# Performance work log

Measured on AMD Instinct MI355X. Metric: run time of the kernel, lower is better.

The kernel has to match this reference:

```python
import jax, jax.numpy as jnp
import numpy as np

POOL_D, POOL_H, POOL_W = 4, 7, 7
SPATIAL_SCALE = 0.25
SAMPLING_RATIO = 2


def setup_inputs() -> dict:
    key = jax.random.key(0)
    k1, k2, k3, k4 = jax.random.split(key, 4)
    N, C, D, H, W = 2, 128, 32, 64, 64
    features = jax.random.normal(k1, (N, C, D, H, W), dtype=jnp.float32)
    R = 256
    inv = 1.0 / SPATIAL_SCALE  # rois live in image coords; features at stride 4
    batch = jax.random.randint(k2, (R,), 0, N).astype(jnp.float32)
    dims = jnp.array([D, H, W], dtype=jnp.float32)
    starts = jax.random.uniform(k3, (R, 3)) * dims * inv * 0.6
    sizes = (0.1 + 0.3 * jax.random.uniform(k4, (R, 3))) * dims * inv
    z1, y1, x1 = starts[:, 0], starts[:, 1], starts[:, 2]
    z2, y2, x2 = z1 + sizes[:, 0], y1 + sizes[:, 1], x1 + sizes[:, 2]
    # roi layout: (batch_idx, x1, y1, z1, x2, y2, z2)
    rois = jnp.stack([batch, x1, y1, z1, x2, y2, z2], axis=1).astype(jnp.float32)
    return {"features": features, "rois": rois}


def _axis(coords, size):
    # classic RoIAlign border handling: outside [-1, size] -> 0 contribution
    valid = (coords >= -1.0) & (coords <= float(size))
    c = jnp.clip(coords, 0.0, float(size) - 1.0)
    lo = jnp.floor(c)
    hi = jnp.minimum(lo + 1.0, float(size) - 1.0)
    w = c - lo  # weight of the hi corner
    return lo.astype(jnp.int32), hi.astype(jnp.int32), w, valid


def roi_align_3d(features, rois):
    N, C, D, H, W = features.shape
    R = rois.shape[0]
    sr = SAMPLING_RATIO
    b = rois[:, 0].astype(jnp.int32)
    x1 = rois[:, 1] * SPATIAL_SCALE
    y1 = rois[:, 2] * SPATIAL_SCALE
    z1 = rois[:, 3] * SPATIAL_SCALE
    x2 = rois[:, 4] * SPATIAL_SCALE
    y2 = rois[:, 5] * SPATIAL_SCALE
    z2 = rois[:, 6] * SPATIAL_SCALE
    rd = jnp.maximum(z2 - z1, 1.0)
    rh = jnp.maximum(y2 - y1, 1.0)
    rw = jnp.maximum(x2 - x1, 1.0)

    def sample_coords(start, extent, P):
        # sampling_ratio sample centers per output bin -> [R, P*sr]
        t = (jnp.arange(P * sr, dtype=jnp.float32) + 0.5) / sr
        return start[:, None] + t[None, :] * (extent / P)[:, None]

    zs = sample_coords(z1, rd, POOL_D)  # [R, SD]
    ys = sample_coords(y1, rh, POOL_H)  # [R, SH]
    xs = sample_coords(x1, rw, POOL_W)  # [R, SW]
    zlo, zhi, wz, vz = _axis(zs, D)
    ylo, yhi, wy, vy = _axis(ys, H)
    xlo, xhi, wx, vx = _axis(xs, W)

    B = b[:, None, None, None]
    Z = lambda a: a[:, :, None, None]
    Y = lambda a: a[:, None, :, None]
    X = lambda a: a[:, None, None, :]

    def g(zi, yi, xi):
        # gather -> [R, SD, SH, SW, C]
        return features[B, :, Z(zi), Y(yi), X(xi)]

    wz1, wy1, wx1 = Z(wz)[..., None], Y(wy)[..., None], X(wx)[..., None]
    wz0, wy0, wx0 = 1.0 - wz1, 1.0 - wy1, 1.0 - wx1
    val = (g(zlo, ylo, xlo) * (wz0 * wy0 * wx0)
           + g(zlo, ylo, xhi) * (wz0 * wy0 * wx1)
           + g(zlo, yhi, xlo) * (wz0 * wy1 * wx0)
           + g(zlo, yhi, xhi) * (wz0 * wy1 * wx1)
           + g(zhi, ylo, xlo) * (wz1 * wy0 * wx0)
           + g(zhi, ylo, xhi) * (wz1 * wy0 * wx1)
           + g(zhi, yhi, xlo) * (wz1 * wy1 * wx0)
           + g(zhi, yhi, xhi) * (wz1 * wy1 * wx1))
    valid = (Z(vz) & Y(vy) & X(vx))[..., None]
    val = jnp.where(valid, val, 0.0)
    # average the sr^3 samples per bin
    val = val.reshape(R, POOL_D, sr, POOL_H, sr, POOL_W, sr, C)
    out = val.mean(axis=(2, 4, 6))  # [R, PD, PH, PW, C]
    return jnp.transpose(out, (0, 4, 1, 2, 3))  # [R, C, PD, PH, PW]


def reference(features, rois):
    return roi_align_3d(features, rois)
```

## Files before the change

### kernel.cpp

```cpp
#include <hip/hip_runtime.h>

constexpr int C_  = 128;
constexpr int D_  = 32;
constexpr int H_  = 64;
constexpr int W_  = 64;
constexpr int PD = 4;
constexpr int PH = 7;
constexpr int PW = 7;
constexpr int SR = 2;
constexpr float SCALE = 0.25f;
constexpr int S_ = D_ * H_ * W_;
constexpr int BINS_PER_ROI = PD * PH * PW;
constexpr int SLAB = PH * PW;

typedef float vf4 __attribute__((ext_vector_type(4)));
typedef float f32x2 __attribute__((ext_vector_type(2)));

__device__ __forceinline__ void axis2(float start, float extent, int P, int p,
                                      int size, int lo[2], int hi[2],
                                      float w[2], bool v[2]) {
    float bin = extent / (float)P;
#pragma unroll
    for (int u = 0; u < 2; ++u) {
        float t = ((float)(p * SR + u) + 0.5f) / (float)SR;
        float coord = start + t * bin;
        v[u] = (coord >= -1.0f) && (coord <= (float)size);
        float cc = fminf(fmaxf(coord, 0.0f), (float)size - 1.0f);
        float fl = floorf(cc);
        lo[u] = (int)fl;
        hi[u] = min(lo[u] + 1, size - 1);
        w[u] = cc - fl;
    }
}

struct AxisW {
    int base;
    float w[4];
};

__device__ __forceinline__ AxisW axis_merge(float start, float extent, int P,
                                            int p, int size) {
    const float bin = extent / (float)P;
    const float t0 = ((float)(p * SR) + 0.5f) / (float)SR;
    const float c0 = start + t0 * bin;
    const float va = (c0 >= -1.0f && c0 <= (float)size) ? 1.0f : 0.0f;
    const float cc0 = fminf(fmaxf(c0, 0.0f), (float)size - 1.0f);
    const float fl0 = floorf(cc0);
    const int lo0 = (int)fl0;
    const int hi0 = min(lo0 + 1, size - 1);
    const float f0 = cc0 - fl0;
    const float a0 = (1.0f - f0) * va;
    const float a1 = f0 * va;
    const float t1 = ((float)(p * SR + 1) + 0.5f) / (float)SR;
    const float c1 = start + t1 * bin;
    const float vb = (c1 >= -1.0f && c1 <= (float)size) ? 1.0f : 0.0f;
    const float cc1 = fminf(fmaxf(c1, 0.0f), (float)size - 1.0f);
    const float fl1 = floorf(cc1);
    const int lo1 = (int)fl1;
    const int hi1 = min(lo1 + 1, size - 1);
    const float f1 = cc1 - fl1;
    const float b0 = (1.0f - f1) * vb;
    const float b1 = f1 * vb;

    const int dh0 = hi0 - lo0;
    const int dl1 = lo1 - lo0;
    const int dh1 = hi1 - lo0;

    float w0 = a0, w1 = 0.f, w2 = 0.f, w3 = 0.f;
    if (dh0 == 0) w0 += a1; else w1 += a1;
    w0 += (dl1 == 0) ? b0 : 0.f;
    w1 += (dl1 == 1) ? b0 : 0.f;
    w2 += (dl1 == 2) ? b0 : 0.f;
    w0 += (dh1 == 0) ? b1 : 0.f;
    w1 += (dh1 == 1) ? b1 : 0.f;
    w2 += (dh1 == 2) ? b1 : 0.f;
    w3 += (dh1 == 3) ? b1 : 0.f;

    AxisW r;
    r.base = lo0;
    r.w[0] = w0; r.w[1] = w1; r.w[2] = w2; r.w[3] = w3;
    return r;
}

__device__ __forceinline__ unsigned int f2bf(float f) {
    unsigned int u = __float_as_uint(f);
    u += 0x7fffu + ((u >> 16) & 1u);
    return u >> 16;
}

__global__ __launch_bounds__(512) void transpose_bf16(
    const float* __restrict__ in, unsigned int* __restrict__ outp) {
    __shared__ unsigned int tileu[256][64];
    const int n  = blockIdx.y;
    const int s0 = blockIdx.x * 256;
    const int t  = threadIdx.x;

    const float* src = in + (size_t)n * C_ * S_;
    unsigned int* dst = outp + (size_t)n * (C_ / 2) * S_;

    if (n == 0 && blockIdx.x == 0 && t < 256) {
        outp[(size_t)gridDim.y * (C_ / 2) * S_ + t] = 0u;
    }

    {
        const int sl  = t & 63;
        const int cp0 = t >> 6;
#pragma unroll
        for (int p = 0; p < 8; ++p) {
            const int cp = cp0 + 8 * p;
            const int c = cp * 2;
            const vf4 a = __builtin_nontemporal_load(
                (const vf4*)&src[(size_t)c * S_ + (s0 + 4 * sl)]);
            const vf4 b = __builtin_nontemporal_load(
                (const vf4*)&src[(size_t)(c + 1) * S_ + (s0 + 4 * sl)]);
            const int col = cp ^ (sl & 31);
            tileu[4 * sl + 0][col] = f2bf(a.x) | (f2bf(b.x) << 16);
            tileu[4 * sl + 1][col] = f2bf(a.y) | (f2bf(b.y) << 16);
            tileu[4 * sl + 2][col] = f2bf(a.z) | (f2bf(b.z) << 16);
            tileu[4 * sl + 3][col] = f2bf(a.w) | (f2bf(b.w) << 16);
        }
    }
    __syncthreads();
    {
        const int cp2   = (t & 31) * 2;
        const int rbase = t >> 5;
#pragma unroll
        for (int it = 0; it < 16; ++it) {
            const int s = rbase + 16 * it;
            const int w = (s >> 2) & 31;
            uint2 v;
            v.x = tileu[s][cp2 ^ w];
            v.y = tileu[s][(cp2 + 1) ^ w];
            *(uint2*)&dst[(size_t)(s0 + s) * (C_ / 2) + cp2] = v;
        }
    }
}

__global__ __launch_bounds__(448, 7) void roi_align_slot(
    const unsigned short* __restrict__ ft,
    const float* __restrict__ rois,
    float* __restrict__ out,
    int R) {
    __shared__ float tile[7][128];

    int roi, pd, part;
    {
        const int B = blockIdx.x;
        if ((R & 7) == 0) {
            const int xcd = B & 7;
            const int j = B >> 3;
            roi = xcd + 8 * (j / 28);
            const int sub = j % 28;
            pd = sub / 7;
            part = sub - pd * 7;
        } else {
            roi = B / 28;
            const int sub = B - roi * 28;
            pd = sub / 7;
            part = sub - pd * 7;
        }
    }

    const int t = threadIdx.x;
    const int w = t >> 6;
    const int lane = t & 63;
    const int slot = part * 7 + w;

    const float* roip = rois + (size_t)roi * 7;
    const int b = (int)roip[0];
    const float x1 = roip[1] * SCALE, y1 = roip[2] * SCALE, z1 = roip[3] * SCALE;
    const float x2 = roip[4] * SCALE, y2 = roip[5] * SCALE, z2 = roip[6] * SCALE;
    const float rd = fmaxf(z2 - z1, 1.0f);
    const float rh = fmaxf(y2 - y1, 1.0f);
    const float rw = fmaxf(x2 - x1, 1.0f);

    AxisW az = axis_merge(z1, rd, PD, pd, D_);
    {
        const float s = 1.0f / (SR * SR * SR);
        az.w[0] *= s; az.w[1] *= s; az.w[2] *= s; az.w[3] *= s;
    }

    const int ph = slot / PW;
    const int pw = slot - ph * PW;
    const AxisW ay = axis_merge(y1, rh, PH, ph, H_);
    const AxisW ax = axis_merge(x1, rw, PW, pw, W_);

    int zw[4], yw[4];
#pragma unroll
    for (int i = 0; i < 4; ++i) {
        zw[i] = __builtin_amdgcn_readfirstlane((int)__float_as_uint(az.w[i]));
        yw[i] = __builtin_amdgcn_readfirstlane((int)__float_as_uint(ay.w[i]));
    }

    const int v = lane >> 4;
    float wxl = ax.w[0];
    wxl = (v == 1) ? ax.w[1] : wxl;
    wxl = (v == 2) ? ax.w[2] : wxl;
    wxl = (v == 3) ? ax.w[3] : wxl;

    unsigned yoff[4];
#pragma unroll
    for (int iy = 0; iy < 4; ++iy) {
        const int yy = min(ay.base + iy, H_ - 1);
        yoff[iy] = ((unsigned)yy * W_ + (unsigned)ax.base) * C_;
    }
    unsigned zrow[4];
#pragma unroll
    for (int iz = 0; iz < 4; ++iz) {
        const int zz = min(az.base + iz, D_ - 1);
        zrow[iz] = (((unsigned)b * D_ + (unsigned)zz) * H_) *
                   (unsigned)(W_ * C_);
    }

    const unsigned short* lanep = ft + (unsigned)lane * 8;

    f32x2 acc2[4];
#pragma unroll
    for (int j = 0; j < 4; ++j) { acc2[j].x = 0.f; acc2[j].y = 0.f; }

    uint4 q[8];
#pragma unroll
    for (int zb = 0; zb < 2; ++zb) {
        if (zb == 1) {
            __builtin_amdgcn_sched_barrier(0);
        }
#pragma unroll
        for (int dz = 0; dz < 2; ++dz) {
            const int iz = 2 * zb + dz;
            if (zw[iz] == 0) continue;
#pragma unroll
            for (int iy = 0; iy < 4; ++iy) {
                if (yw[iy] == 0) continue;
                q[dz * 4 + iy] = *(const uint4*)(lanep + zrow[iz] + yoff[iy]);
            }
        }
#pragma unroll
        for (int dz = 0; dz < 2; ++dz) {
            const int iz = 2 * zb + dz;
            if (zw[iz] == 0) continue;
#pragma unroll
            for (int iy = 0; iy < 4; ++iy) {
                if (yw[iy] == 0) continue;
                const float wf = (az.w[iz] * ay.w[iy]) * wxl;
                f32x2 wf2; wf2.x = wf; wf2.y = wf;
                const uint4 qq = q[dz * 4 + iy];
                f32x2 p;
                p.x = __uint_as_float(qq.x << 16);
                p.y = __uint_as_float(qq.x & 0xffff0000u);
                acc2[0] = __builtin_elementwise_fma(p, wf2, acc2[0]);
                p.x = __uint_as_float(qq.y << 16);
                p.y = __uint_as_float(qq.y & 0xffff0000u);
                acc2[1] = __builtin_elementwise_fma(p, wf2, acc2[1]);
                p.x = __uint_as_float(qq.z << 16);
                p.y = __uint_as_float(qq.z & 0xffff0000u);
                acc2[2] = __builtin_elementwise_fma(p, wf2, acc2[2]);
                p.x = __uint_as_float(qq.w << 16);
                p.y = __uint_as_float(qq.w & 0xffff0000u);
                acc2[3] = __builtin_elementwise_fma(p, wf2, acc2[3]);
            }
        }
    }

#pragma unroll
    for (int j = 0; j < 4; ++j) {
        float sx = acc2[j].x;
        sx += __shfl_xor(sx, 16);
        sx += __shfl_xor(sx, 32);
        float sy = acc2[j].y;
        sy += __shfl_xor(sy, 16);
        sy += __shfl_xor(sy, 32);
        if (lane < 16) {
            tile[w][lane * 8 + 2 * j]     = sx;
            tile[w][lane * 8 + 2 * j + 1] = sy;
        }
    }

    __syncthreads();

    const size_t obase =
        (size_t)roi * C_ * BINS_PER_ROI + (size_t)pd * SLAB + (size_t)part * 7;
#pragma unroll
    for (int it = 0; it < 2; ++it) {
        const int idx = t + it * 448;
        const int c = idx / 7;
        const int o = idx - c * 7;
        __builtin_nontemporal_store(tile[o][c],
                                    &out[obase + (size_t)c * BINS_PER_ROI + o]);
    }
}

__global__ void roi_align_direct(const float* __restrict__ feat,
                                 const float* __restrict__ rois,
                                 float* __restrict__ out, int total) {
    const int tid = blockIdx.x * blockDim.x + threadIdx.x;
    if (tid >= total) return;
    int t = tid;
    const int pw = t % PW; t /= PW;
    const int ph = t % PH; t /= PH;
    const int pd = t % PD; t /= PD;
    const int c = t % C_;  t /= C_;
    const int r = t;

    const float* roi = rois + (size_t)r * 7;
    const int b = (int)roi[0];
    const float x1 = roi[1] * SCALE, y1 = roi[2] * SCALE, z1 = roi[3] * SCALE;
    const float x2 = roi[4] * SCALE, y2 = roi[5] * SCALE, z2 = roi[6] * SCALE;
    const float rd = fmaxf(z2 - z1, 1.0f);
    const float rh = fmaxf(y2 - y1, 1.0f);
    const float rw = fmaxf(x2 - x1, 1.0f);

    int zlo[2], zhi[2], ylo[2], yhi[2], xlo[2], xhi[2];
    float wz[2], wy[2], wx[2];
    bool vz[2], vy[2], vx[2];
    axis2(z1, rd, PD, pd, D_, zlo, zhi, wz, vz);
    axis2(y1, rh, PH, ph, H_, ylo, yhi, wy, vy);
    axis2(x1, rw, PW, pw, W_, xlo, xhi, wx, vx);

    const float* fc = feat + ((size_t)b * C_ + c) * S_;
    float acc = 0.0f;
#pragma unroll
    for (int i = 0; i < 2; ++i) {
        if (!vz[i]) continue;
#pragma unroll
        for (int j = 0; j < 2; ++j) {
            if (!vy[j]) continue;
            const size_t r00 = ((size_t)zlo[i] * H_ + ylo[j]) * W_;
            const size_t r10 = ((size_t)zhi[i] * H_ + ylo[j]) * W_;
            const size_t r01 = ((size_t)zlo[i] * H_ + yhi[j]) * W_;
            const size_t r11 = ((size_t)zhi[i] * H_ + yhi[j]) * W_;
            const float wz1 = wz[i], wz0 = 1.0f - wz1;
            const float wy1 = wy[j], wy0 = 1.0f - wy1;
#pragma unroll
            for (int k = 0; k < 2; ++k) {
                if (!vx[k]) continue;
                const float wx1 = wx[k], wx0 = 1.0f - wx1;
                acc += wz0 * (wy0 * (wx0 * fc[r00 + xlo[k]] + wx1 * fc[r00 + xhi[k]]) +
                              wy1 * (wx0 * fc[r01 + xlo[k]] + wx1 * fc[r01 + xhi[k]])) +
                       wz1 * (wy0 * (wx0 * fc[r10 + xlo[k]] + wx1 * fc[r10 + xhi[k]]) +
                              wy1 * (wx0 * fc[r11 + xlo[k]] + wx1 * fc[r11 + xhi[k]]));
            }
        }
    }
    out[tid] = acc * (1.0f / (SR * SR * SR));
}

extern "C" void kernel_launch(void* const* d_in, const int* in_sizes, int n_in,
                              void* d_out, int out_size, void* d_ws,
                              size_t ws_size, hipStream_t stream) {
    const float* features = (const float*)d_in[0];
    const float* rois = (const float*)d_in[1];
    float* out = (float*)d_out;

    const int R = in_sizes[1] / 7;
    const int N = in_sizes[0] / (C_ * S_);
    const size_t need = (size_t)in_sizes[0] * sizeof(unsigned short) + 1024;

    if (ws_size >= need) {
        unsigned short* ft = (unsigned short*)d_ws;

        dim3 tg(S_ / 256, N);
        transpose_bf16<<<tg, 512, 0, stream>>>(features, (unsigned int*)ft);

        roi_align_slot<<<R * PD * 7, 448, 0, stream>>>(ft, rois, out, R);
    } else {
        const int total = R * C_ * BINS_PER_ROI;
        roi_align_direct<<<(total + 255) / 256, 256, 0, stream>>>(
            features, rois, out, total);
    }
}
```

Measured before the change: 251.1 us.

## Process a full PH×PW slab per block, looping over ph inside each wave

Each block now handles a whole (roi, pd) slab of 49 bins, and each wave loops over all 7 ph rows for a fixed pw column, instead of one block per 7 bins. The grid shrinks by a factor of seven, the per-block roi and z-axis setup is shared across more work, and output stores become contiguous 49-float runs per channel. The cost is fewer blocks (1024) with more serial work per wave and a larger shared tile, which may reduce latency hiding for the gather loads. The transpose kernel is unchanged and still runs every call.

Measured after the change: 284.0 us. +13.1%, slower.

```diff
diff --git a/kernel.cpp b/kernel.cpp
--- a/kernel.cpp
+++ b/kernel.cpp
@@ -38,9 +38,8 @@
     float w[4];
 };
 
-__device__ __forceinline__ AxisW axis_merge(float start, float extent, int P,
-                                            int p, int size) {
-    const float bin = extent / (float)P;
+__device__ __forceinline__ AxisW axis_merge_bin(float start, float bin, int p,
+                                                int size) {
     const float t0 = ((float)(p * SR) + 0.5f) / (float)SR;
     const float c0 = start + t0 * bin;
     const float va = (c0 >= -1.0f && c0 <= (float)size) ? 1.0f : 0.0f;
@@ -82,6 +81,11 @@
     return r;
 }
 
+__device__ __forceinline__ AxisW axis_merge(float start, float extent, int P,
+                                            int p, int size) {
+    return axis_merge_bin(start, extent / (float)P, p, size);
+}
+
 __device__ __forceinline__ unsigned int f2bf(float f) {
     unsigned int u = __float_as_uint(f);
     u += 0x7fffu + ((u >> 16) & 1u);
@@ -136,35 +140,30 @@
     }
 }
 
-__global__ __launch_bounds__(448, 7) void roi_align_slot(
+__global__ __launch_bounds__(448, 7) void roi_align_slab7(
     const unsigned short* __restrict__ ft,
     const float* __restrict__ rois,
     float* __restrict__ out,
     int R) {
-    __shared__ float tile[7][128];
-
-    int roi, pd, part;
+    __shared__ float tile[SLAB][132];
+
+    int roi, pd;
     {
         const int B = blockIdx.x;
         if ((R & 7) == 0) {
             const int xcd = B & 7;
             const int j = B >> 3;
-            roi = xcd + 8 * (j / 28);
-            const int sub = j % 28;
-            pd = sub / 7;
-            part = sub - pd * 7;
+            roi = xcd + 8 * (j >> 2);
+            pd = j & 3;
         } else {
-            roi = B / 28;
-            const int sub = B - roi * 28;
-            pd = sub / 7;
-            part = sub - pd * 7;
+            roi = B >> 2;
+            pd = B & 3;
         }
     }
 
     const int t = threadIdx.x;
     const int w = t >> 6;
     const int lane = t & 63;
-    const int slot = part * 7 + w;
 
     const float* roip = rois + (size_t)roi * 7;
     const int b = (int)roip[0];
@@ -179,18 +178,13 @@
         const float s = 1.0f / (SR * SR * SR);
         az.w[0] *= s; az.w[1] *= s; az.w[2] *= s; az.w[3] *= s;
     }
-
-    const int ph = slot / PW;
-    const int pw = slot - ph * PW;
-    const AxisW ay = axis_merge(y1, rh, PH, ph, H_);
-    const AxisW ax = axis_merge(x1, rw, PW, pw, W_);
-
-    int zw[4], yw[4];
-#pragma unroll
-    for (int i = 0; i < 4; ++i) {
+    const AxisW ax = axis_merge(x1, rw, PW, w, W_);
+    const float biny = rh / (float)PH;
+
+    int zw[4];
+#pragma unroll
+    for (int i = 0; i < 4; ++i)
         zw[i] = __builtin_amdgcn_readfirstlane((int)__float_as_uint(az.w[i]));
-        yw[i] = __builtin_amdgcn_readfirstlane((int)__float_as_uint(ay.w[i]));
-    }
 
     const int v = lane >> 4;
     float wxl = ax.w[0];
@@ -198,12 +192,6 @@
     wxl = (v == 2) ? ax.w[2] : wxl;
     wxl = (v == 3) ? ax.w[3] : wxl;
 
-    unsigned yoff[4];
-#pragma unroll
-    for (int iy = 0; iy < 4; ++iy) {
-        const int yy = min(ay.base + iy, H_ - 1);
-        yoff[iy] = ((unsigned)yy * W_ + (unsigned)ax.base) * C_;
-    }
     unsigned zrow[4];
 #pragma unroll
     for (int iz = 0; iz < 4; ++iz) {
@@ -214,76 +202,91 @@
 
     const unsigned short* lanep = ft + (unsigned)lane * 8;
 
-    f32x2 acc2[4];
-#pragma unroll
-    for (int j = 0; j < 4; ++j) { acc2[j].x = 0.f; acc2[j].y = 0.f; }
-
-    uint4 q[8];
-#pragma unroll
-    for (int zb = 0; zb < 2; ++zb) {
-        if (zb == 1) {
-            __builtin_amdgcn_sched_barrier(0);
-        }
-#pragma unroll
-        for (int dz = 0; dz < 2; ++dz) {
-            const int iz = 2 * zb + dz;
-            if (zw[iz] == 0) continue;
-#pragma unroll
-            for (int iy = 0; iy < 4; ++iy) {
-                if (yw[iy] == 0) continue;
-                q[dz * 4 + iy] = *(const uint4*)(lanep + zrow[iz] + yoff[iy]);
+#pragma unroll
+    for (int ph = 0; ph < PH; ++ph) {
+        const AxisW ay = axis_merge_bin(y1, biny, ph, H_);
+        int yw[4];
+#pragma unroll
+        for (int i = 0; i < 4; ++i)
+            yw[i] = __builtin_amdgcn_readfirstlane(
+                (int)__float_as_uint(ay.w[i]));
+        unsigned yoff[4];
+#pragma unroll
+        for (int iy = 0; iy < 4; ++iy) {
+            const int yy = min(ay.base + iy, H_ - 1);
+            yoff[iy] = ((unsigned)yy * W_ + (unsigned)ax.base) * C_;
+        }
+
+        f32x2 acc2[4];
+#pragma unroll
+        for (int j = 0; j < 4; ++j) { acc2[j].x = 0.f; acc2[j].y = 0.f; }
+
+        uint4 q[8];
+#pragma unroll
+        for (int zb = 0; zb < 2; ++zb) {
+            if (zb == 1) __builtin_amdgcn_sched_barrier(0);
+#pragma unroll
+            for (int dz = 0; dz < 2; ++dz) {
+                const int iz = 2 * zb + dz;
+                if (zw[iz] == 0) continue;
+#pragma unroll
+                for (int iy = 0; iy < 4; ++iy) {
+                    if (yw[iy] == 0) continue;
+                    q[dz * 4 + iy] =
+                        *(const uint4*)(lanep + zrow[iz] + yoff[iy]);
+                }
             }
-        }
-#pragma unroll
-        for (int dz = 0; dz < 2; ++dz) {
-            const int iz = 2 * zb + dz;
-            if (zw[iz] == 0) continue;
-#pragma unroll
-            for (int iy = 0; iy < 4; ++iy) {
-                if (yw[iy] == 0) continue;
-                const float wf = (az.w[iz] * ay.w[iy]) * wxl;
-                f32x2 wf2; wf2.x = wf; wf2.y = wf;
-                const uint4 qq = q[dz * 4 + iy];
-                f32x2 p;
-                p.x = __uint_as_float(qq.x << 16);
-                p.y = __uint_as_float(qq.x & 0xffff0000u);
-                acc2[0] = __builtin_elementwise_fma(p, wf2, acc2[0]);
-                p.x = __uint_as_float(qq.y << 16);
-                p.y = __uint_as_float(qq.y & 0xffff0000u);
-                acc2[1] = __builtin_elementwise_fma(p, wf2, acc2[1]);
-                p.x = __uint_as_float(qq.z << 16);
-                p.y = __uint_as_float(qq.z & 0xffff0000u);
-                acc2[2] = __builtin_elementwise_fma(p, wf2, acc2[2]);
-                p.x = __uint_as_float(qq.w << 16);
-                p.y = __uint_as_float(qq.w & 0xffff0000u);
-                acc2[3] = __builtin_elementwise_fma(p, wf2, acc2[3]);
+#pragma unroll
+            for (int dz = 0; dz < 2; ++dz) {
+                const int iz = 2 * zb + dz;
+                if (zw[iz] == 0) continue;
+#pragma unroll
+                for (int iy = 0; iy < 4; ++iy) {
+                    if (yw[iy] == 0) continue;
+                    const float wf = (az.w[iz] * ay.w[iy]) * wxl;
+                    f32x2 wf2; wf2.x = wf; wf2.y = wf;
+                    const uint4 qq = q[dz * 4 + iy];
+                    f32x2 p;
+                    p.x = __uint_as_float(qq.x << 16);
+                    p.y = __uint_as_float(qq.x & 0xffff0000u);
+                    acc2[0] = __builtin_elementwise_fma(p, wf2, acc2[0]);
+                    p.x = __uint_as_float(qq.y << 16);
+                    p.y = __uint_as_float(qq.y & 0xffff0000u);
+                    acc2[1] = __builtin_elementwise_fma(p, wf2, acc2[1]);
+                    p.x = __uint_as_float(qq.z << 16);
+                    p.y = __uint_as_float(qq.z & 0xffff0000u);
+                    acc2[2] = __builtin_elementwise_fma(p, wf2, acc2[2]);
+                    p.x = __uint_as_float(qq.w << 16);
+                    p.y = __uint_as_float(qq.w & 0xffff0000u);
+                    acc2[3] = __builtin_elementwise_fma(p, wf2, acc2[3]);
+                }
             }
         }
-    }
-
-#pragma unroll
-    for (int j = 0; j < 4; ++j) {
-        float sx = acc2[j].x;
-        sx += __shfl_xor(sx, 16);
-        sx += __shfl_xor(sx, 32);
-        float sy = acc2[j].y;
-        sy += __shfl_xor(sy, 16);
-        sy += __shfl_xor(sy, 32);
-        if (lane < 16) {
-            tile[w][lane * 8 + 2 * j]     = sx;
-            tile[w][lane * 8 + 2 * j + 1] = sy;
+
+        const int slot = ph * PW + w;
+#pragma unroll
+        for (int j = 0; j < 4; ++j) {
+            float sx = acc2[j].x;
+            sx += __shfl_xor(sx, 16);
+            sx += __shfl_xor(sx, 32);
+            float sy = acc2[j].y;
+            sy += __shfl_xor(sy, 16);
+            sy += __shfl_xor(sy, 32);
+            if (lane < 16) {
+                tile[slot][lane * 8 + 2 * j]     = sx;
+                tile[slot][lane * 8 + 2 * j + 1] = sy;
+            }
         }
     }
 
     __syncthreads();
 
-    const size_t obase =
-        (size_t)roi * C_ * BINS_PER_ROI + (size_t)pd * SLAB + (size_t)part * 7;
-#pragma unroll
-    for (int it = 0; it < 2; ++it) {
+    const size_t obase = (size_t)roi * C_ * BINS_PER_ROI + (size_t)pd * SLAB;
+#pragma unroll
+    for (int it = 0; it < 14; ++it) {
         const int idx = t + it * 448;
-        const int c = idx / 7;
-        const int o = idx - c * 7;
+        const int c = idx / SLAB;
+        const int o = idx - c * SLAB;
         __builtin_nontemporal_store(tile[o][c],
                                     &out[obase + (size_t)c * BINS_PER_ROI + o]);
     }
@@ -361,7 +364,7 @@
         dim3 tg(S_ / 256, N);
         transpose_bf16<<<tg, 512, 0, stream>>>(features, (unsigned int*)ft);
 
-        roi_align_slot<<<R * PD * 7, 448, 0, stream>>>(ft, rois, out, R);
+        roi_align_slab7<<<R * PD, 448, 0, stream>>>(ft, rois, out, R);
     } else {
         const int total = R * C_ * BINS_PER_ROI;
         roi_align_direct<<<(total + 255) / 256, 256, 0, stream>>>(
```
